# Kernel optimization log

Hardware: AMD Instinct MI355X
Metric: run time of the kernel (lower is better)

## Reference

```python
import jax, jax.numpy as jnp
import numpy as np

N = 100000   # nodes
E = 3200000  # edges
M = 4096     # moves
K = 16       # orders per move
NEG_SLOPE = 0.2  # PyG GATv2Conv default negative_slope

PARAM_SHAPES = {
    'g1_Wl': (10, 15), 'g1_Wr': (10, 15), 'g1_att': (10,), 'g1_b': (10,),
    'g2_Wl': (10, 25), 'g2_Wr': (10, 25), 'g2_att': (10,), 'g2_b': (10,),
    'g3_Wl': (10, 25), 'g3_Wr': (10, 25), 'g3_att': (10,), 'g3_b': (10,),
    'vt_W': (20, 29), 'vt_b': (20,), 'va_W': (1, 20), 'va_b': (1,),
    'vv_W': (10, 20), 'vv_b': (10,), 'vl_W': (1, 10), 'vl_b': (1,),
    'at_W': (20, 48), 'at_b': (20,), 'dt_W': (20, 23), 'dt_b': (20,),
    'oa_W': (1, 20), 'oa_b': (1,), 'ov_W': (1, 20), 'ov_b': (1,),
}
PARAM_NAMES = list(PARAM_SHAPES.keys())


def _linear(x, W, b):
    return x @ W.T + b


def _gatv2(x, src, dst, Wl, Wr, att, b):
    # GATv2Conv (heads=1, self-loops appended by caller), eval mode (no dropout)
    xl = x @ Wl.T  # messages from source nodes
    xr = x @ Wr.T
    e = (jax.nn.leaky_relu(xl[src] + xr[dst], NEG_SLOPE) * att).sum(-1)  # [E+N]
    emax = jax.ops.segment_max(e, dst, num_segments=N)
    ee = jnp.exp(e - emax[dst])
    denom = jax.ops.segment_sum(ee, dst, num_segments=N)
    alpha = ee / denom[dst]
    return jax.ops.segment_sum(alpha[:, None] * xl[src], dst, num_segments=N) + b


def _forward(x1, x2, edges, move_src, move_dst, move_armies, is_attack, params):
    (g1_Wl, g1_Wr, g1_att, g1_b,
     g2_Wl, g2_Wr, g2_att, g2_b,
     g3_Wl, g3_Wr, g3_att, g3_b,
     vt_W, vt_b, va_W, va_b, vv_W, vv_b, vl_W, vl_b,
     at_W, at_b, dt_W, dt_b, oa_W, oa_b, ov_W, ov_b) = params
    x2t = jnp.tile(x2, (N, 1))  # [N,4]
    self_idx = jnp.arange(N, dtype=edges.dtype)
    src = jnp.concatenate([edges[0], self_idx])
    dst = jnp.concatenate([edges[1], self_idx])
    x = jax.nn.relu(_gatv2(x1, src, dst, g1_Wl, g1_Wr, g1_att, g1_b))
    x = jax.nn.relu(_gatv2(jnp.concatenate([x, x1], 1), src, dst, g2_Wl, g2_Wr, g2_att, g2_b))
    x = jax.nn.relu(_gatv2(jnp.concatenate([x, x1], 1), src, dst, g3_Wl, g3_Wr, g3_att, g3_b))  # [N,10]
    # per-move order tensors (vectorized over [M,K]); deploy uses move_src as target
    xs, xd = x[move_src], x[move_dst]       # [M,K,10]
    x1s, x1d = x1[move_src], x1[move_dst]   # [M,K,15]
    extra = 0.6 * move_armies - 0.7 * (x1d[..., 3] + x1d[..., 4])
    attack_in = jnp.concatenate([xs, xd, x1s[..., 3:], x1d[..., 1:],
                                 move_armies[..., None], extra[..., None]], -1)  # [M,K,48]
    deploy_in = jnp.concatenate([xs, x1s[..., 3:], move_armies[..., None]], -1)  # [M,K,23]
    feat = jnp.where(is_attack[..., None] == 1,
                     _linear(attack_in, at_W, at_b),
                     _linear(deploy_in, dt_W, dt_b))
    feat = jax.nn.relu(feat)  # dropout = identity (eval)
    attn = jax.nn.softmax(_linear(feat, oa_W, oa_b), axis=1)  # softmax over orders
    p = (attn * _linear(feat, ov_W, ov_b)).sum(axis=(1, 2))   # [M]
    # value head: attention pooling over all nodes
    Vn = jax.nn.relu(_linear(jnp.concatenate([x, x1, x2t], 1), vt_W, vt_b))  # [N,20]
    vatt = jax.nn.softmax(_linear(Vn, va_W, va_b), axis=0)
    Vp = jax.nn.relu((vatt * _linear(Vn, vv_W, vv_b)).sum(axis=0))
    V = jnp.tanh(_linear(Vp, vl_W, vl_b))[0]
    return V, jax.nn.log_softmax(p, axis=0)


def setup_inputs() -> dict:
    key = jax.random.key(0)
    ks = iter(jax.random.split(key, 64))
    inp = {
        'x1': jax.random.normal(next(ks), (N, 15), jnp.float32),
        'x2': jax.random.normal(next(ks), (4,), jnp.float32),
        'edges': jax.random.randint(next(ks), (2, E), 0, N, jnp.int32),
        'move_src': jax.random.randint(next(ks), (M, K), 0, N, jnp.int32),
        'move_dst': jax.random.randint(next(ks), (M, K), 0, N, jnp.int32),
        'move_armies': jax.random.uniform(next(ks), (M, K), jnp.float32) * 10.0,
        'is_attack': jax.random.randint(next(ks), (M, K), 0, 2, jnp.int32),
    }
    for name, shape in PARAM_SHAPES.items():
        inp[name] = jax.random.normal(next(ks), shape, jnp.float32) * 0.1
    return inp


def reference(x1, x2, edges, move_src, move_dst, move_armies, is_attack,
              g1_Wl, g1_Wr, g1_att, g1_b, g2_Wl, g2_Wr, g2_att, g2_b,
              g3_Wl, g3_Wr, g3_att, g3_b, vt_W, vt_b, va_W, va_b,
              vv_W, vv_b, vl_W, vl_b, at_W, at_b, dt_W, dt_b,
              oa_W, oa_b, ov_W, ov_b):
    params = (g1_Wl, g1_Wr, g1_att, g1_b, g2_Wl, g2_Wr, g2_att, g2_b,
              g3_Wl, g3_Wr, g3_att, g3_b, vt_W, vt_b, va_W, va_b,
              vv_W, vv_b, vl_W, vl_b, at_W, at_b, dt_W, dt_b,
              oa_W, oa_b, ov_W, ov_b)
    return _forward(x1, x2, edges, move_src, move_dst, move_armies, is_attack, params)
```

## Files before the change

### kernel.cpp

```cpp
#include <hip/hip_runtime.h>
#include <hip/hip_bf16.h>
#include <hip/hip_fp16.h>
#include <math.h>

#define NN 100000
#define NE 3200000
#define MM 4096
#define KK 16
#define NEG_SLOPE 0.2f
#define SUB 8
#define BSH 8
#define NB 391
#define PCH 4096
#define FCAP 9728
#define XS 12
#define XSH 16

__device__ __forceinline__ void h10_to_f(const uint4& w0, unsigned w2, float* xs) {
    float2 f;
    f = __half22float2(*(const __half2*)&w0.x); xs[0]=f.x; xs[1]=f.y;
    f = __half22float2(*(const __half2*)&w0.y); xs[2]=f.x; xs[3]=f.y;
    f = __half22float2(*(const __half2*)&w0.z); xs[4]=f.x; xs[5]=f.y;
    f = __half22float2(*(const __half2*)&w0.w); xs[6]=f.x; xs[7]=f.y;
    f = __half22float2(*(const __half2*)&w2);   xs[8]=f.x; xs[9]=f.y;
}

__global__ __launch_bounds__(1024) void partition_kernel(const int* __restrict__ edges,
                                                         int* __restrict__ cnt,
                                                         unsigned* __restrict__ recs) {
    __shared__ unsigned rl[PCH];
    __shared__ unsigned srt[PCH];
    __shared__ unsigned short bb[PCH];
    __shared__ unsigned short bbs[PCH];
    __shared__ int h[NB];
    __shared__ int sc[1024];
    __shared__ int lb[NB];
    __shared__ int gb[NB];
    __shared__ int cur[NB];
    const int total = NE + NN;
    int base = blockIdx.x * PCH;
    int n = min(PCH, total - base);
    int t = threadIdx.x;
    if (t < NB) { h[t] = 0; cur[t] = 0; }
    __syncthreads();
    for (int j = t; j < n; j += 1024) {
        int i = base + j;
        int s, d;
        if (i < NE) { s = edges[i]; d = edges[NE + i]; }
        else        { s = i - NE; d = s; }
        rl[j] = ((unsigned)(d & 255) << 17) | (unsigned)s;
        int b = d >> BSH;
        bb[j] = (unsigned short)b;
        atomicAdd(&h[b], 1);
    }
    __syncthreads();
    int hv = (t < NB) ? h[t] : 0;
    sc[t] = hv;
    __syncthreads();
    for (int off = 1; off < 1024; off <<= 1) {
        int v = (t >= off) ? sc[t - off] : 0;
        __syncthreads();
        sc[t] += v;
        __syncthreads();
    }
    if (t < NB) {
        lb[t] = sc[t] - hv;
        if (hv > 0) gb[t] = atomicAdd(&cnt[t], hv);
    }
    __syncthreads();
    for (int j = t; j < n; j += 1024) {
        int b = bb[j];
        int l = atomicAdd(&cur[b], 1);
        int dst = lb[b] + l;
        srt[dst] = rl[j];
        bbs[dst] = (unsigned short)b;
    }
    __syncthreads();
    for (int j = t; j < n; j += 1024) {
        int b = bbs[j];
        int pos = gb[b] + (j - lb[b]);
        if (pos < FCAP) recs[(long)b * FCAP + pos] = srt[j];
    }
}

__global__ void bucket_scan_kernel(const int* __restrict__ cnt, int* __restrict__ bbase) {
    __shared__ int part[512];
    int t = threadIdx.x;
    int c = (t < NB) ? min(cnt[t], FCAP) : 0;
    part[t] = c;
    __syncthreads();
    for (int off = 1; off < 512; off <<= 1) {
        int v = (t >= off) ? part[t - off] : 0;
        __syncthreads();
        part[t] += v;
        __syncthreads();
    }
    if (t < NB) bbase[t] = part[t] - c;
    if (t == NB - 1) bbase[NB] = part[t];
}

__global__ __launch_bounds__(1024) void fine_sort_kernel(const unsigned* __restrict__ recs,
                                                         const int* __restrict__ cnt,
                                                         const int* __restrict__ bbase,
                                                         int* __restrict__ csr_src,
                                                         int* __restrict__ offsets) {
    __shared__ unsigned rl[FCAP];
    __shared__ int hist[256];
    __shared__ int sc[256];
    __shared__ int hb[257];
    __shared__ int cur[256];
    int b = blockIdx.x;
    int beg = bbase[b];
    int nb = min(cnt[b], FCAP);
    int t = threadIdx.x;
    int nodebase = b << BSH;
    int nnodes = min(256, NN - nodebase);
    if (t < 256) { hist[t] = 0; cur[t] = 0; }
    __syncthreads();
    const unsigned* rsrc = recs + (long)b * FCAP;
    for (int j = t; j < nb; j += 1024) {
        unsigned r = rsrc[j];
        rl[j] = r;
        atomicAdd(&hist[r >> 17], 1);
    }
    __syncthreads();
    int hv = (t < 256) ? hist[t] : 0;
    if (t < 256) sc[t] = hv;
    __syncthreads();
    for (int off = 1; off < 256; off <<= 1) {
        int v = 0;
        if (t < 256 && t >= off) v = sc[t - off];
        __syncthreads();
        if (t < 256) sc[t] += v;
        __syncthreads();
    }
    if (t < 256) hb[t] = sc[t] - hv;
    if (t == 0) hb[256] = nb;
    __syncthreads();
    for (int j = t; j < nb; j += 1024) {
        unsigned r = rl[j];
        int l = r >> 17;
        int p = hb[l] + atomicAdd(&cur[l], 1);
        csr_src[beg + p] = (int)(r & 0x1FFFFu);
    }
    if (t < nnodes) offsets[nodebase + t] = beg + hb[t];
    if (b == NB - 1 && t == 0) offsets[NN] = beg + nb;
}

__global__ void linear1_kernel(const float* __restrict__ x1,
                               const float* __restrict__ Wl,
                               const float* __restrict__ Wr,
                               __half* __restrict__ xlh,
                               float* __restrict__ xr) {
    int i = blockIdx.x * blockDim.x + threadIdx.x;
    if (i >= NN) return;
    float in[15];
    #pragma unroll
    for (int j = 0; j < 15; j++) in[j] = x1[i * 15 + j];
    float sl[10];
    #pragma unroll
    for (int o = 0; o < 10; o++) {
        float l = 0.f, r = 0.f;
        #pragma unroll
        for (int j = 0; j < 15; j++) {
            l += Wl[o * 15 + j] * in[j];
            r += Wr[o * 15 + j] * in[j];
        }
        sl[o] = l;
        xr[(long)i * XS + o] = r;
    }
    unsigned u[5];
    #pragma unroll
    for (int q = 0; q < 5; q++) {
        __half2 hh = __floats2half2_rn(sl[2*q], sl[2*q+1]);
        u[q] = *(unsigned*)&hh;
    }
    uint4* p4 = (uint4*)(xlh + (long)i * XSH);
    p4[0] = make_uint4(u[0], u[1], u[2], u[3]);
    *(uint2*)(xlh + (long)i * XSH + 8) = make_uint2(u[4], 0u);
}

template<bool FUSE_NEXT>
__global__ void gat_aggregate_kernel(const int* __restrict__ csr_src,
                                     const int* __restrict__ offsets,
                                     const __half* __restrict__ xlh,
                                     const float* __restrict__ xr,
                                     const float* __restrict__ att,
                                     const float* __restrict__ b,
                                     const float* __restrict__ x1,
                                     const float* __restrict__ nWl,
                                     const float* __restrict__ nWr,
                                     __half* __restrict__ xlo,
                                     float* __restrict__ xro,
                                     float* __restrict__ xout)
{
    int t = blockIdx.x * blockDim.x + threadIdx.x;
    int node = t / SUB;
    int lane = t % SUB;
    if (node >= NN) return;
    float xrn[12], a[10];
    const float4* xr4 = (const float4*)(xr + (long)node * XS);
    #pragma unroll
    for (int q = 0; q < 3; q++) {
        float4 v = xr4[q];
        xrn[4*q] = v.x; xrn[4*q+1] = v.y; xrn[4*q+2] = v.z; xrn[4*q+3] = v.w;
    }
    #pragma unroll
    for (int h = 0; h < 10; h++) a[h] = att[h];
    int beg = offsets[node], end = offsets[node + 1];
    float den = 0.f, num[10];
    #pragma unroll
    for (int h = 0; h < 10; h++) num[h] = 0.f;
    int j = beg + lane;
    for (; j + 3 * SUB < end; j += 4 * SUB) {
        int s0 = csr_src[j];
        int s1 = csr_src[j + SUB];
        int s2 = csr_src[j + 2 * SUB];
        int s3 = csr_src[j + 3 * SUB];
        const __half *p0 = xlh + (long)s0 * XSH, *p1 = xlh + (long)s1 * XSH;
        const __half *p2 = xlh + (long)s2 * XSH, *p3 = xlh + (long)s3 * XSH;
        uint4 w0a = *(const uint4*)p0; unsigned w0b = *(const unsigned*)(p0 + 8);
        uint4 w1a = *(const uint4*)p1; unsigned w1b = *(const unsigned*)(p1 + 8);
        uint4 w2a = *(const uint4*)p2; unsigned w2b = *(const unsigned*)(p2 + 8);
        uint4 w3a = *(const uint4*)p3; unsigned w3b = *(const unsigned*)(p3 + 8);
        uint4 wa[4] = {w0a, w1a, w2a, w3a};
        unsigned wb[4] = {w0b, w1b, w2b, w3b};
        #pragma unroll
        for (int q = 0; q < 4; q++) {
            float xs[10];
            h10_to_f(wa[q], wb[q], xs);
            float e = 0.f;
            #pragma unroll
            for (int h = 0; h < 10; h++) {
                float v = xs[h] + xrn[h];
                v = (v >= 0.f) ? v : NEG_SLOPE * v;
                e += v * a[h];
            }
            float w = __expf(e);
            den += w;
            #pragma unroll
            for (int h = 0; h < 10; h++) num[h] += w * xs[h];
        }
    }
    for (; j < end; j += SUB) {
        int s = csr_src[j];
        const __half* ph = xlh + (long)s * XSH;
        uint4 wa = *(const uint4*)ph;
        unsigned wb = *(const unsigned*)(ph + 8);
        float xs[10];
        h10_to_f(wa, wb, xs);
        float e = 0.f;
        #pragma unroll
        for (int h = 0; h < 10; h++) {
            float v = xs[h] + xrn[h];
            v = (v >= 0.f) ? v : NEG_SLOPE * v;
            e += v * a[h];
        }
        float w = __expf(e);
        den += w;
        #pragma unroll
        for (int h = 0; h < 10; h++) num[h] += w * xs[h];
    }
    #pragma unroll
    for (int off = SUB / 2; off; off >>= 1) {
        den += __shfl_xor(den, off, SUB);
        #pragma unroll
        for (int h = 0; h < 10; h++) num[h] += __shfl_xor(num[h], off, SUB);
    }
    float inv = 1.f / den;
    float xo[10];
    #pragma unroll
    for (int h = 0; h < 10; h++) xo[h] = fmaxf(num[h] * inv + b[h], 0.f);
    if (FUSE_NEXT) {
        if (lane < 5) {
            float in2[25];
            #pragma unroll
            for (int h = 0; h < 10; h++) in2[h] = xo[h];
            #pragma unroll
            for (int h = 0; h < 15; h++) in2[10 + h] = x1[(long)node * 15 + h];
            int o0 = 2 * lane, o1 = 2 * lane + 1;
            float sl0 = 0.f, sl1 = 0.f, sr0 = 0.f, sr1 = 0.f;
            #pragma unroll
            for (int jj = 0; jj < 25; jj++) {
                sl0 += nWl[o0 * 25 + jj] * in2[jj];
                sl1 += nWl[o1 * 25 + jj] * in2[jj];
                sr0 += nWr[o0 * 25 + jj] * in2[jj];
                sr1 += nWr[o1 * 25 + jj] * in2[jj];
            }
            __half2 hp = __floats2half2_rn(sl0, sl1);
            *(unsigned*)(xlo + (long)node * XSH + o0) = *(unsigned*)&hp;
            *(float2*)(xro + (long)node * XS + o0) = make_float2(sr0, sr1);
        }
    } else {
        if (lane == 0) {
            #pragma unroll
            for (int h = 0; h < 10; h++) xout[(long)node * XS + h] = xo[h];
        }
    }
}

__global__ void move_kernel(const float* __restrict__ x,
                            const float* __restrict__ x1,
                            const int* __restrict__ msrc,
                            const int* __restrict__ mdst,
                            const float* __restrict__ armies,
                            const int* __restrict__ isatk,
                            const float* __restrict__ at_W, const float* __restrict__ at_b,
                            const float* __restrict__ dt_W, const float* __restrict__ dt_b,
                            const float* __restrict__ oa_W, const float* __restrict__ oa_b,
                            const float* __restrict__ ov_W, const float* __restrict__ ov_b,
                            float* __restrict__ p) {
    int t = blockIdx.x * blockDim.x + threadIdx.x;
    int m = t >> 4;
    int k = t & 15;
    int s = msrc[t], d = mdst[t];
    float arm = armies[t];
    bool atk = (isatk[t] == 1);
    float xsrc[12];
    const float4* xs4 = (const float4*)(x + (long)s * XS);
    #pragma unroll
    for (int q = 0; q < 3; q++) {
        float4 v = xs4[q];
        xsrc[4*q] = v.x; xsrc[4*q+1] = v.y; xsrc[4*q+2] = v.z; xsrc[4*q+3] = v.w;
    }
    float feat[20];
    if (atk) {
        float in[48];
        #pragma unroll
        for (int h = 0; h < 10; h++) in[h] = xsrc[h];
        const float4* xd4 = (const float4*)(x + (long)d * XS);
        float xdst[12];
        #pragma unroll
        for (int q = 0; q < 3; q++) {
            float4 v = xd4[q];
            xdst[4*q] = v.x; xdst[4*q+1] = v.y; xdst[4*q+2] = v.z; xdst[4*q+3] = v.w;
        }
        #pragma unroll
        for (int h = 0; h < 10; h++) in[10 + h] = xdst[h];
        #pragma unroll
        for (int h = 0; h < 12; h++) in[20 + h] = x1[(long)s * 15 + 3 + h];
        #pragma unroll
        for (int h = 0; h < 14; h++) in[32 + h] = x1[(long)d * 15 + 1 + h];
        in[46] = arm;
        in[47] = 0.6f * arm - 0.7f * (x1[(long)d * 15 + 3] + x1[(long)d * 15 + 4]);
        #pragma unroll
        for (int o = 0; o < 20; o++) {
            float sum = at_b[o];
            #pragma unroll
            for (int j = 0; j < 48; j++) sum += at_W[o * 48 + j] * in[j];
            feat[o] = fmaxf(sum, 0.f);
        }
    } else {
        float in[23];
        #pragma unroll
        for (int h = 0; h < 10; h++) in[h] = xsrc[h];
        #pragma unroll
        for (int h = 0; h < 12; h++) in[10 + h] = x1[(long)s * 15 + 3 + h];
        in[22] = arm;
        #pragma unroll
        for (int o = 0; o < 20; o++) {
            float sum = dt_b[o];
            #pragma unroll
            for (int j = 0; j < 23; j++) sum += dt_W[o * 23 + j] * in[j];
            feat[o] = fmaxf(sum, 0.f);
        }
    }
    float oa = oa_b[0], ov = ov_b[0];
    #pragma unroll
    for (int j = 0; j < 20; j++) {
        oa += oa_W[j] * feat[j];
        ov += ov_W[j] * feat[j];
    }
    float mx = oa;
    #pragma unroll
    for (int off = 8; off; off >>= 1) mx = fmaxf(mx, __shfl_xor(mx, off, 16));
    float w = __expf(oa - mx);
    float nume = w * ov;
    float den = w;
    #pragma unroll
    for (int off = 8; off; off >>= 1) {
        nume += __shfl_xor(nume, off, 16);
        den  += __shfl_xor(den,  off, 16);
    }
    if (k == 0) p[m] = nume / den;
}

__global__ void logsoftmax_kernel(const float* __restrict__ p, float* __restrict__ out) {
    __shared__ float sm[256];
    int tid = threadIdx.x;
    float mx = -INFINITY;
    for (int i = tid; i < MM; i += 256) mx = fmaxf(mx, p[i]);
    sm[tid] = mx; __syncthreads();
    for (int s = 128; s; s >>= 1) { if (tid < s) sm[tid] = fmaxf(sm[tid], sm[tid + s]); __syncthreads(); }
    mx = sm[0]; __syncthreads();
    float sum = 0.f;
    for (int i = tid; i < MM; i += 256) sum += expf(p[i] - mx);
    sm[tid] = sum; __syncthreads();
    for (int s = 128; s; s >>= 1) { if (tid < s) sm[tid] += sm[tid + s]; __syncthreads(); }
    float ls = mx + logf(sm[0]);
    for (int i = tid; i < MM; i += 256) out[i] = p[i] - ls;
}

__global__ void value12_kernel(const float* __restrict__ x,
                               const float* __restrict__ x1,
                               const float* __restrict__ x2,
                               const float* __restrict__ vt_W, const float* __restrict__ vt_b,
                               const float* __restrict__ va_W, const float* __restrict__ va_b,
                               const float* __restrict__ vv_W, const float* __restrict__ vv_b,
                               float* __restrict__ partials) {
    __shared__ float sm[4][11];
    int i = blockIdx.x * blockDim.x + threadIdx.x;
    float w = 0.f;
    float acc[10];
    #pragma unroll
    for (int h = 0; h < 10; h++) acc[h] = 0.f;
    if (i < NN) {
        float in[29];
        const float4* xi4 = (const float4*)(x + (long)i * XS);
        float xi[12];
        #pragma unroll
        for (int q = 0; q < 3; q++) {
            float4 v = xi4[q];
            xi[4*q] = v.x; xi[4*q+1] = v.y; xi[4*q+2] = v.z; xi[4*q+3] = v.w;
        }
        #pragma unroll
        for (int h = 0; h < 10; h++) in[h] = xi[h];
        #pragma unroll
        for (int h = 0; h < 15; h++) in[10 + h] = x1[(long)i * 15 + h];
        #pragma unroll
        for (int h = 0; h < 4; h++) in[25 + h] = x2[h];
        float Vn[20];
        #pragma unroll
        for (int o = 0; o < 20; o++) {
            float s = vt_b[o];
            #pragma unroll
            for (int j = 0; j < 29; j++) s += vt_W[o * 29 + j] * in[j];
            Vn[o] = fmaxf(s, 0.f);
        }
        float lg = va_b[0];
        #pragma unroll
        for (int j = 0; j < 20; j++) lg += va_W[j] * Vn[j];
        w = __expf(lg);
        #pragma unroll
        for (int o = 0; o < 10; o++) {
            float s = vv_b[o];
            #pragma unroll
            for (int j = 0; j < 20; j++) s += vv_W[o * 20 + j] * Vn[j];
            acc[o] = w * s;
        }
    }
    #pragma unroll
    for (int off = 32; off; off >>= 1) {
        w += __shfl_xor(w, off, 64);
        #pragma unroll
        for (int h = 0; h < 10; h++) acc[h] += __shfl_xor(acc[h], off, 64);
    }
    int wid = threadIdx.x >> 6;
    if ((threadIdx.x & 63) == 0) {
        #pragma unroll
        for (int h = 0; h < 10; h++) sm[wid][h] = acc[h];
        sm[wid][10] = w;
    }
    __syncthreads();
    if (threadIdx.x < 11) {
        int c = threadIdx.x;
        partials[(long)blockIdx.x * 12 + c] = sm[0][c] + sm[1][c] + sm[2][c] + sm[3][c];
    }
}

__global__ void value3_kernel(const float* __restrict__ partials, int nparts,
                              const float* __restrict__ vl_W, const float* __restrict__ vl_b,
                              float* __restrict__ out0) {
    int lane = threadIdx.x;
    float s[11];
    #pragma unroll
    for (int c = 0; c < 11; c++) s[c] = 0.f;
    for (int j = lane; j < nparts; j += 64)
        #pragma unroll
        for (int c = 0; c < 11; c++) s[c] += partials[(long)j * 12 + c];
    #pragma unroll
    for (int off = 32; off; off >>= 1)
        #pragma unroll
        for (int c = 0; c < 11; c++) s[c] += __shfl_xor(s[c], off, 64);
    if (lane == 0) {
        float inv = 1.0f / s[10];
        float v = vl_b[0];
        #pragma unroll
        for (int h = 0; h < 10; h++) v += vl_W[h] * fmaxf(s[h] * inv, 0.f);
        out0[0] = tanhf(v);
    }
}

extern "C" void kernel_launch(void* const* d_in, const int* in_sizes, int n_in,
                              void* d_out, int out_size, void* d_ws, size_t ws_size,
                              hipStream_t stream) {
    const float* x1      = (const float*)d_in[0];
    const float* x2      = (const float*)d_in[1];
    const int*   edges   = (const int*)d_in[2];
    const int*   msrc    = (const int*)d_in[3];
    const int*   mdst    = (const int*)d_in[4];
    const float* armies  = (const float*)d_in[5];
    const int*   isatk   = (const int*)d_in[6];
    const float* g1_Wl = (const float*)d_in[7],  *g1_Wr = (const float*)d_in[8];
    const float* g1_att= (const float*)d_in[9],  *g1_b  = (const float*)d_in[10];
    const float* g2_Wl = (const float*)d_in[11], *g2_Wr = (const float*)d_in[12];
    const float* g2_att= (const float*)d_in[13], *g2_b  = (const float*)d_in[14];
    const float* g3_Wl = (const float*)d_in[15], *g3_Wr = (const float*)d_in[16];
    const float* g3_att= (const float*)d_in[17], *g3_b  = (const float*)d_in[18];
    const float* vt_W  = (const float*)d_in[19], *vt_b  = (const float*)d_in[20];
    const float* va_W  = (const float*)d_in[21], *va_b  = (const float*)d_in[22];
    const float* vv_W  = (const float*)d_in[23], *vv_b  = (const float*)d_in[24];
    const float* vl_W  = (const float*)d_in[25], *vl_b  = (const float*)d_in[26];
    const float* at_W  = (const float*)d_in[27], *at_b  = (const float*)d_in[28];
    const float* dt_W  = (const float*)d_in[29], *dt_b  = (const float*)d_in[30];
    const float* oa_W  = (const float*)d_in[31], *oa_b  = (const float*)d_in[32];
    const float* ov_W  = (const float*)d_in[33], *ov_b  = (const float*)d_in[34];

    float* out = (float*)d_out;

    float* ws = (float*)d_ws;
    __half* xlhA = (__half*)ws;
    __half* xlhB = xlhA + (long)NN * XSH;
    float* xrA = (float*)(xlhB + (long)NN * XSH);
    float* xrB = xrA + (long)NN * XS;
    float* xF  = xrB + (long)NN * XS;
    int* csr_src = (int*)(xF + (long)NN * XS);
    int* offsets = csr_src + (NE + NN);
    unsigned* recs = (unsigned*)(offsets + NN + 4);
    int* cnt   = (int*)(recs + (long)NB * FCAP);
    int* bbase = cnt + NB + 1;
    float* pbuf = (float*)(bbase + NB + 3);
    float* partials = pbuf + MM;

    const int nodeBlocks = (NN + 255) / 256;
    const int aggBlocks  = ((long)NN * SUB + 255) / 256;
    const int partBlocks = (NE + NN + PCH - 1) / PCH;

    hipMemsetAsync(cnt, 0, NB * sizeof(int), stream);
    partition_kernel<<<partBlocks, 1024, 0, stream>>>(edges, cnt, recs);
    bucket_scan_kernel<<<1, 512, 0, stream>>>(cnt, bbase);
    fine_sort_kernel<<<NB, 1024, 0, stream>>>(recs, cnt, bbase, csr_src, offsets);

    linear1_kernel<<<nodeBlocks, 256, 0, stream>>>(x1, g1_Wl, g1_Wr, xlhA, xrA);
    gat_aggregate_kernel<true><<<aggBlocks, 256, 0, stream>>>(
        csr_src, offsets, xlhA, xrA, g1_att, g1_b, x1, g2_Wl, g2_Wr, xlhB, xrB, nullptr);
    gat_aggregate_kernel<true><<<aggBlocks, 256, 0, stream>>>(
        csr_src, offsets, xlhB, xrB, g2_att, g2_b, x1, g3_Wl, g3_Wr, xlhA, xrA, nullptr);
    gat_aggregate_kernel<false><<<aggBlocks, 256, 0, stream>>>(
        csr_src, offsets, xlhA, xrA, g3_att, g3_b, x1, nullptr, nullptr, nullptr, nullptr, xF);

    move_kernel<<<(MM * KK) / 256, 256, 0, stream>>>(
        xF, x1, msrc, mdst, armies, isatk,
        at_W, at_b, dt_W, dt_b, oa_W, oa_b, ov_W, ov_b, pbuf);
    logsoftmax_kernel<<<1, 256, 0, stream>>>(pbuf, out + 1);

    value12_kernel<<<nodeBlocks, 256, 0, stream>>>(
        xF, x1, x2, vt_W, vt_b, va_W, va_b, vv_W, vv_b, partials);
    value3_kernel<<<1, 64, 0, stream>>>(partials, nodeBlocks, vl_W, vl_b, out);
}
```

Before: 377.7 us.

## Fuse all stages into one cooperative persistent kernel with grid syncs

Replaces the chain of separate kernel launches (partition, scan, fine sort, linear, three GAT aggregations, move scoring, log-softmax, value head) with a single cooperative mega-kernel. It uses grid-stride loops over a fixed grid and grid.sync between stages, and a shared-memory union reused across phases. The aim is to remove per-launch overhead and inter-kernel gaps. In exchange, parallelism is capped at 256 blocks of 1024 threads, the 1024-thread blocks may hurt occupancy in the aggregation phases, and each grid barrier costs time.

```diff
diff --git a/kernel.cpp b/kernel.cpp
--- a/kernel.cpp
+++ b/kernel.cpp
@@ -1,7 +1,9 @@
 #include <hip/hip_runtime.h>
-#include <hip/hip_bf16.h>
+#include <hip/hip_cooperative_groups.h>
 #include <hip/hip_fp16.h>
 #include <math.h>
+
+namespace cg = cooperative_groups;
 
 #define NN 100000
 #define NE 3200000
@@ -15,6 +17,38 @@
 #define FCAP 9728
 #define XS 12
 #define XSH 16
+#define GRID 256
+#define TPB 1024
+#define GSIZE (GRID * TPB)
+#define VPAD 100032
+
+struct KParams {
+    const float *x1, *x2;
+    const int *edges, *msrc, *mdst;
+    const float *armies; const int *isatk;
+    const float *g1_Wl, *g1_Wr, *g1_att, *g1_b;
+    const float *g2_Wl, *g2_Wr, *g2_att, *g2_b;
+    const float *g3_Wl, *g3_Wr, *g3_att, *g3_b;
+    const float *vt_W, *vt_b, *va_W, *va_b, *vv_W, *vv_b, *vl_W, *vl_b;
+    const float *at_W, *at_b, *dt_W, *dt_b, *oa_W, *oa_b, *ov_W, *ov_b;
+    __half *xlhA, *xlhB; float *xrA, *xrB, *xF;
+    int *csr_src, *offsets, *cnt, *bbase;
+    unsigned *recs;
+    float *pbuf, *partials, *out;
+};
+
+union SMem {
+    struct {
+        unsigned rl[PCH]; unsigned srt[PCH];
+        unsigned short bb[PCH]; unsigned short bbs[PCH];
+        int h[NB]; int sc[TPB]; int lb[NB]; int gb[NB]; int cur[NB];
+    } part;
+    struct {
+        unsigned rl[FCAP]; int hist[256]; int sc[256]; int hb[257]; int cur[256];
+    } fine;
+    struct { int part[TPB]; } scan;
+    struct { float sm[TPB]; } red;
+};
 
 __device__ __forceinline__ void h10_to_f(const uint4& w0, unsigned w2, float* xs) {
     float2 f;
@@ -25,210 +59,72 @@
     f = __half22float2(*(const __half2*)&w2);   xs[8]=f.x; xs[9]=f.y;
 }
 
-__global__ __launch_bounds__(1024) void partition_kernel(const int* __restrict__ edges,
-                                                         int* __restrict__ cnt,
-                                                         unsigned* __restrict__ recs) {
-    __shared__ unsigned rl[PCH];
-    __shared__ unsigned srt[PCH];
-    __shared__ unsigned short bb[PCH];
-    __shared__ unsigned short bbs[PCH];
-    __shared__ int h[NB];
-    __shared__ int sc[1024];
-    __shared__ int lb[NB];
-    __shared__ int gb[NB];
-    __shared__ int cur[NB];
-    const int total = NE + NN;
-    int base = blockIdx.x * PCH;
-    int n = min(PCH, total - base);
-    int t = threadIdx.x;
-    if (t < NB) { h[t] = 0; cur[t] = 0; }
-    __syncthreads();
-    for (int j = t; j < n; j += 1024) {
-        int i = base + j;
-        int s, d;
-        if (i < NE) { s = edges[i]; d = edges[NE + i]; }
-        else        { s = i - NE; d = s; }
-        rl[j] = ((unsigned)(d & 255) << 17) | (unsigned)s;
-        int b = d >> BSH;
-        bb[j] = (unsigned short)b;
-        atomicAdd(&h[b], 1);
-    }
-    __syncthreads();
-    int hv = (t < NB) ? h[t] : 0;
-    sc[t] = hv;
-    __syncthreads();
-    for (int off = 1; off < 1024; off <<= 1) {
-        int v = (t >= off) ? sc[t - off] : 0;
-        __syncthreads();
-        sc[t] += v;
-        __syncthreads();
-    }
-    if (t < NB) {
-        lb[t] = sc[t] - hv;
-        if (hv > 0) gb[t] = atomicAdd(&cnt[t], hv);
-    }
-    __syncthreads();
-    for (int j = t; j < n; j += 1024) {
-        int b = bb[j];
-        int l = atomicAdd(&cur[b], 1);
-        int dst = lb[b] + l;
-        srt[dst] = rl[j];
-        bbs[dst] = (unsigned short)b;
-    }
-    __syncthreads();
-    for (int j = t; j < n; j += 1024) {
-        int b = bbs[j];
-        int pos = gb[b] + (j - lb[b]);
-        if (pos < FCAP) recs[(long)b * FCAP + pos] = srt[j];
-    }
-}
-
-__global__ void bucket_scan_kernel(const int* __restrict__ cnt, int* __restrict__ bbase) {
-    __shared__ int part[512];
-    int t = threadIdx.x;
-    int c = (t < NB) ? min(cnt[t], FCAP) : 0;
-    part[t] = c;
-    __syncthreads();
-    for (int off = 1; off < 512; off <<= 1) {
-        int v = (t >= off) ? part[t - off] : 0;
-        __syncthreads();
-        part[t] += v;
-        __syncthreads();
-    }
-    if (t < NB) bbase[t] = part[t] - c;
-    if (t == NB - 1) bbase[NB] = part[t];
-}
-
-__global__ __launch_bounds__(1024) void fine_sort_kernel(const unsigned* __restrict__ recs,
-                                                         const int* __restrict__ cnt,
-                                                         const int* __restrict__ bbase,
-                                                         int* __restrict__ csr_src,
-                                                         int* __restrict__ offsets) {
-    __shared__ unsigned rl[FCAP];
-    __shared__ int hist[256];
-    __shared__ int sc[256];
-    __shared__ int hb[257];
-    __shared__ int cur[256];
-    int b = blockIdx.x;
-    int beg = bbase[b];
-    int nb = min(cnt[b], FCAP);
-    int t = threadIdx.x;
-    int nodebase = b << BSH;
-    int nnodes = min(256, NN - nodebase);
-    if (t < 256) { hist[t] = 0; cur[t] = 0; }
-    __syncthreads();
-    const unsigned* rsrc = recs + (long)b * FCAP;
-    for (int j = t; j < nb; j += 1024) {
-        unsigned r = rsrc[j];
-        rl[j] = r;
-        atomicAdd(&hist[r >> 17], 1);
-    }
-    __syncthreads();
-    int hv = (t < 256) ? hist[t] : 0;
-    if (t < 256) sc[t] = hv;
-    __syncthreads();
-    for (int off = 1; off < 256; off <<= 1) {
-        int v = 0;
-        if (t < 256 && t >= off) v = sc[t - off];
-        __syncthreads();
-        if (t < 256) sc[t] += v;
-        __syncthreads();
-    }
-    if (t < 256) hb[t] = sc[t] - hv;
-    if (t == 0) hb[256] = nb;
-    __syncthreads();
-    for (int j = t; j < nb; j += 1024) {
-        unsigned r = rl[j];
-        int l = r >> 17;
-        int p = hb[l] + atomicAdd(&cur[l], 1);
-        csr_src[beg + p] = (int)(r & 0x1FFFFu);
-    }
-    if (t < nnodes) offsets[nodebase + t] = beg + hb[t];
-    if (b == NB - 1 && t == 0) offsets[NN] = beg + nb;
-}
-
-__global__ void linear1_kernel(const float* __restrict__ x1,
-                               const float* __restrict__ Wl,
-                               const float* __restrict__ Wr,
-                               __half* __restrict__ xlh,
-                               float* __restrict__ xr) {
-    int i = blockIdx.x * blockDim.x + threadIdx.x;
-    if (i >= NN) return;
-    float in[15];
-    #pragma unroll
-    for (int j = 0; j < 15; j++) in[j] = x1[i * 15 + j];
-    float sl[10];
-    #pragma unroll
-    for (int o = 0; o < 10; o++) {
-        float l = 0.f, r = 0.f;
-        #pragma unroll
-        for (int j = 0; j < 15; j++) {
-            l += Wl[o * 15 + j] * in[j];
-            r += Wr[o * 15 + j] * in[j];
-        }
-        sl[o] = l;
-        xr[(long)i * XS + o] = r;
-    }
-    unsigned u[5];
-    #pragma unroll
-    for (int q = 0; q < 5; q++) {
-        __half2 hh = __floats2half2_rn(sl[2*q], sl[2*q+1]);
-        u[q] = *(unsigned*)&hh;
-    }
-    uint4* p4 = (uint4*)(xlh + (long)i * XSH);
-    p4[0] = make_uint4(u[0], u[1], u[2], u[3]);
-    *(uint2*)(xlh + (long)i * XSH + 8) = make_uint2(u[4], 0u);
-}
-
-template<bool FUSE_NEXT>
-__global__ void gat_aggregate_kernel(const int* __restrict__ csr_src,
-                                     const int* __restrict__ offsets,
-                                     const __half* __restrict__ xlh,
-                                     const float* __restrict__ xr,
-                                     const float* __restrict__ att,
-                                     const float* __restrict__ b,
-                                     const float* __restrict__ x1,
-                                     const float* __restrict__ nWl,
-                                     const float* __restrict__ nWr,
-                                     __half* __restrict__ xlo,
-                                     float* __restrict__ xro,
-                                     float* __restrict__ xout)
-{
-    int t = blockIdx.x * blockDim.x + threadIdx.x;
-    int node = t / SUB;
-    int lane = t % SUB;
-    if (node >= NN) return;
-    float xrn[12], a[10];
-    const float4* xr4 = (const float4*)(xr + (long)node * XS);
-    #pragma unroll
-    for (int q = 0; q < 3; q++) {
-        float4 v = xr4[q];
-        xrn[4*q] = v.x; xrn[4*q+1] = v.y; xrn[4*q+2] = v.z; xrn[4*q+3] = v.w;
-    }
-    #pragma unroll
-    for (int h = 0; h < 10; h++) a[h] = att[h];
-    int beg = offsets[node], end = offsets[node + 1];
-    float den = 0.f, num[10];
-    #pragma unroll
-    for (int h = 0; h < 10; h++) num[h] = 0.f;
-    int j = beg + lane;
-    for (; j + 3 * SUB < end; j += 4 * SUB) {
-        int s0 = csr_src[j];
-        int s1 = csr_src[j + SUB];
-        int s2 = csr_src[j + 2 * SUB];
-        int s3 = csr_src[j + 3 * SUB];
-        const __half *p0 = xlh + (long)s0 * XSH, *p1 = xlh + (long)s1 * XSH;
-        const __half *p2 = xlh + (long)s2 * XSH, *p3 = xlh + (long)s3 * XSH;
-        uint4 w0a = *(const uint4*)p0; unsigned w0b = *(const unsigned*)(p0 + 8);
-        uint4 w1a = *(const uint4*)p1; unsigned w1b = *(const unsigned*)(p1 + 8);
-        uint4 w2a = *(const uint4*)p2; unsigned w2b = *(const unsigned*)(p2 + 8);
-        uint4 w3a = *(const uint4*)p3; unsigned w3b = *(const unsigned*)(p3 + 8);
-        uint4 wa[4] = {w0a, w1a, w2a, w3a};
-        unsigned wb[4] = {w0b, w1b, w2b, w3b};
-        #pragma unroll
-        for (int q = 0; q < 4; q++) {
+template<bool FUSE>
+__device__ void aggregate_phase(const KParams& P,
+                                const __half* __restrict__ xlh,
+                                const float* __restrict__ xr,
+                                const float* __restrict__ att,
+                                const float* __restrict__ bias,
+                                const float* __restrict__ nWl,
+                                const float* __restrict__ nWr,
+                                __half* __restrict__ xlo,
+                                float* __restrict__ xro,
+                                float* __restrict__ xout,
+                                int tid) {
+    for (long wk = tid; wk < (long)NN * SUB; wk += GSIZE) {
+        int node = (int)(wk >> 3);
+        int lane = (int)(wk & 7);
+        float xrn[12], a[10];
+        const float4* xr4 = (const float4*)(xr + (long)node * XS);
+        #pragma unroll
+        for (int q = 0; q < 3; q++) {
+            float4 v = xr4[q];
+            xrn[4*q]=v.x; xrn[4*q+1]=v.y; xrn[4*q+2]=v.z; xrn[4*q+3]=v.w;
+        }
+        #pragma unroll
+        for (int h = 0; h < 10; h++) a[h] = att[h];
+        int beg = P.offsets[node], end = P.offsets[node + 1];
+        float den = 0.f, num[10];
+        #pragma unroll
+        for (int h = 0; h < 10; h++) num[h] = 0.f;
+        int j = beg + lane;
+        for (; j + 3 * SUB < end; j += 4 * SUB) {
+            int s0 = P.csr_src[j];
+            int s1 = P.csr_src[j + SUB];
+            int s2 = P.csr_src[j + 2 * SUB];
+            int s3 = P.csr_src[j + 3 * SUB];
+            const __half *p0 = xlh + (long)s0 * XSH, *p1 = xlh + (long)s1 * XSH;
+            const __half *p2 = xlh + (long)s2 * XSH, *p3 = xlh + (long)s3 * XSH;
+            uint4 w0a = *(const uint4*)p0; unsigned w0b = *(const unsigned*)(p0 + 8);
+            uint4 w1a = *(const uint4*)p1; unsigned w1b = *(const unsigned*)(p1 + 8);
+            uint4 w2a = *(const uint4*)p2; unsigned w2b = *(const unsigned*)(p2 + 8);
+            uint4 w3a = *(const uint4*)p3; unsigned w3b = *(const unsigned*)(p3 + 8);
+            uint4 wa[4] = {w0a, w1a, w2a, w3a};
+            unsigned wb[4] = {w0b, w1b, w2b, w3b};
+            #pragma unroll
+            for (int q = 0; q < 4; q++) {
+                float xs[10];
+                h10_to_f(wa[q], wb[q], xs);
+                float e = 0.f;
+                #pragma unroll
+                for (int h = 0; h < 10; h++) {
+                    float v = xs[h] + xrn[h];
+                    v = (v >= 0.f) ? v : NEG_SLOPE * v;
+                    e += v * a[h];
+                }
+                float w = __expf(e);
+                den += w;
+                #pragma unroll
+                for (int h = 0; h < 10; h++) num[h] += w * xs[h];
+            }
+        }
+        for (; j < end; j += SUB) {
+            int s = P.csr_src[j];
+            const __half* ph = xlh + (long)s * XSH;
+            uint4 wa = *(const uint4*)ph;
+            unsigned wb = *(const unsigned*)(ph + 8);
             float xs[10];
-            h10_to_f(wa[q], wb[q], xs);
+            h10_to_f(wa, wb, xs);
             float e = 0.f;
             #pragma unroll
             for (int h = 0; h < 10; h++) {
@@ -241,320 +137,411 @@
             #pragma unroll
             for (int h = 0; h < 10; h++) num[h] += w * xs[h];
         }
-    }
-    for (; j < end; j += SUB) {
-        int s = csr_src[j];
-        const __half* ph = xlh + (long)s * XSH;
-        uint4 wa = *(const uint4*)ph;
-        unsigned wb = *(const unsigned*)(ph + 8);
-        float xs[10];
-        h10_to_f(wa, wb, xs);
-        float e = 0.f;
-        #pragma unroll
-        for (int h = 0; h < 10; h++) {
-            float v = xs[h] + xrn[h];
-            v = (v >= 0.f) ? v : NEG_SLOPE * v;
-            e += v * a[h];
-        }
-        float w = __expf(e);
-        den += w;
-        #pragma unroll
-        for (int h = 0; h < 10; h++) num[h] += w * xs[h];
-    }
-    #pragma unroll
-    for (int off = SUB / 2; off; off >>= 1) {
-        den += __shfl_xor(den, off, SUB);
-        #pragma unroll
-        for (int h = 0; h < 10; h++) num[h] += __shfl_xor(num[h], off, SUB);
-    }
-    float inv = 1.f / den;
-    float xo[10];
-    #pragma unroll
-    for (int h = 0; h < 10; h++) xo[h] = fmaxf(num[h] * inv + b[h], 0.f);
-    if (FUSE_NEXT) {
-        if (lane < 5) {
-            float in2[25];
-            #pragma unroll
-            for (int h = 0; h < 10; h++) in2[h] = xo[h];
-            #pragma unroll
-            for (int h = 0; h < 15; h++) in2[10 + h] = x1[(long)node * 15 + h];
-            int o0 = 2 * lane, o1 = 2 * lane + 1;
-            float sl0 = 0.f, sl1 = 0.f, sr0 = 0.f, sr1 = 0.f;
-            #pragma unroll
-            for (int jj = 0; jj < 25; jj++) {
-                sl0 += nWl[o0 * 25 + jj] * in2[jj];
-                sl1 += nWl[o1 * 25 + jj] * in2[jj];
-                sr0 += nWr[o0 * 25 + jj] * in2[jj];
-                sr1 += nWr[o1 * 25 + jj] * in2[jj];
-            }
-            __half2 hp = __floats2half2_rn(sl0, sl1);
-            *(unsigned*)(xlo + (long)node * XSH + o0) = *(unsigned*)&hp;
-            *(float2*)(xro + (long)node * XS + o0) = make_float2(sr0, sr1);
-        }
-    } else {
-        if (lane == 0) {
-            #pragma unroll
-            for (int h = 0; h < 10; h++) xout[(long)node * XS + h] = xo[h];
+        #pragma unroll
+        for (int off = SUB / 2; off; off >>= 1) {
+            den += __shfl_xor(den, off, SUB);
+            #pragma unroll
+            for (int h = 0; h < 10; h++) num[h] += __shfl_xor(num[h], off, SUB);
+        }
+        float inv = 1.f / den;
+        float xo[10];
+        #pragma unroll
+        for (int h = 0; h < 10; h++) xo[h] = fmaxf(num[h] * inv + bias[h], 0.f);
+        if (FUSE) {
+            if (lane < 5) {
+                float in2[25];
+                #pragma unroll
+                for (int h = 0; h < 10; h++) in2[h] = xo[h];
+                #pragma unroll
+                for (int h = 0; h < 15; h++) in2[10 + h] = P.x1[(long)node * 15 + h];
+                int o0 = 2 * lane, o1 = 2 * lane + 1;
+                float sl0 = 0.f, sl1 = 0.f, sr0 = 0.f, sr1 = 0.f;
+                #pragma unroll
+                for (int jj = 0; jj < 25; jj++) {
+                    sl0 += nWl[o0 * 25 + jj] * in2[jj];
+                    sl1 += nWl[o1 * 25 + jj] * in2[jj];
+                    sr0 += nWr[o0 * 25 + jj] * in2[jj];
+                    sr1 += nWr[o1 * 25 + jj] * in2[jj];
+                }
+                __half2 hp = __floats2half2_rn(sl0, sl1);
+                *(unsigned*)(xlo + (long)node * XSH + o0) = *(unsigned*)&hp;
+                *(float2*)(xro + (long)node * XS + o0) = make_float2(sr0, sr1);
+            }
+        } else {
+            if (lane == 0) {
+                #pragma unroll
+                for (int h = 0; h < 10; h++) xout[(long)node * XS + h] = xo[h];
+            }
         }
     }
 }
 
-__global__ void move_kernel(const float* __restrict__ x,
-                            const float* __restrict__ x1,
-                            const int* __restrict__ msrc,
-                            const int* __restrict__ mdst,
-                            const float* __restrict__ armies,
-                            const int* __restrict__ isatk,
-                            const float* __restrict__ at_W, const float* __restrict__ at_b,
-                            const float* __restrict__ dt_W, const float* __restrict__ dt_b,
-                            const float* __restrict__ oa_W, const float* __restrict__ oa_b,
-                            const float* __restrict__ ov_W, const float* __restrict__ ov_b,
-                            float* __restrict__ p) {
-    int t = blockIdx.x * blockDim.x + threadIdx.x;
-    int m = t >> 4;
-    int k = t & 15;
-    int s = msrc[t], d = mdst[t];
-    float arm = armies[t];
-    bool atk = (isatk[t] == 1);
-    float xsrc[12];
-    const float4* xs4 = (const float4*)(x + (long)s * XS);
-    #pragma unroll
-    for (int q = 0; q < 3; q++) {
-        float4 v = xs4[q];
-        xsrc[4*q] = v.x; xsrc[4*q+1] = v.y; xsrc[4*q+2] = v.z; xsrc[4*q+3] = v.w;
+__global__ __launch_bounds__(TPB, 4) void mega_kernel(KParams P) {
+    cg::grid_group grid = cg::this_grid();
+    __shared__ SMem sm;
+    int t = threadIdx.x;
+    int tid = blockIdx.x * TPB + t;
+
+    for (int i = tid; i < NB; i += GSIZE) P.cnt[i] = 0;
+    grid.sync();
+
+    {
+        const int total = NE + NN;
+        const int nchunks = (total + PCH - 1) / PCH;
+        for (int c = blockIdx.x; c < nchunks; c += GRID) {
+            int base = c * PCH;
+            int n = min(PCH, total - base);
+            if (t < NB) { sm.part.h[t] = 0; sm.part.cur[t] = 0; }
+            __syncthreads();
+            for (int j = t; j < n; j += TPB) {
+                int i = base + j;
+                int s, d;
+                if (i < NE) { s = P.edges[i]; d = P.edges[NE + i]; }
+                else        { s = i - NE; d = s; }
+                sm.part.rl[j] = ((unsigned)(d & 255) << 17) | (unsigned)s;
+                int b = d >> BSH;
+                sm.part.bb[j] = (unsigned short)b;
+                atomicAdd(&sm.part.h[b], 1);
+            }
+            __syncthreads();
+            int hv = (t < NB) ? sm.part.h[t] : 0;
+            sm.part.sc[t] = hv;
+            __syncthreads();
+            for (int off = 1; off < TPB; off <<= 1) {
+                int v = (t >= off) ? sm.part.sc[t - off] : 0;
+                __syncthreads();
+                sm.part.sc[t] += v;
+                __syncthreads();
+            }
+            if (t < NB) {
+                sm.part.lb[t] = sm.part.sc[t] - hv;
+                if (hv > 0) sm.part.gb[t] = atomicAdd(&P.cnt[t], hv);
+            }
+            __syncthreads();
+            for (int j = t; j < n; j += TPB) {
+                int b = sm.part.bb[j];
+                int l = atomicAdd(&sm.part.cur[b], 1);
+                int dst = sm.part.lb[b] + l;
+                sm.part.srt[dst] = sm.part.rl[j];
+                sm.part.bbs[dst] = (unsigned short)b;
+            }
+            __syncthreads();
+            for (int j = t; j < n; j += TPB) {
+                int b = sm.part.bbs[j];
+                int pos = sm.part.gb[b] + (j - sm.part.lb[b]);
+                if (pos < FCAP) P.recs[(long)b * FCAP + pos] = sm.part.srt[j];
+            }
+            __syncthreads();
+        }
     }
-    float feat[20];
-    if (atk) {
-        float in[48];
-        #pragma unroll
-        for (int h = 0; h < 10; h++) in[h] = xsrc[h];
-        const float4* xd4 = (const float4*)(x + (long)d * XS);
-        float xdst[12];
+    grid.sync();
+
+    if (blockIdx.x == 0) {
+        int c = (t < NB) ? min(P.cnt[t], FCAP) : 0;
+        sm.scan.part[t] = c;
+        __syncthreads();
+        for (int off = 1; off < TPB; off <<= 1) {
+            int v = (t >= off) ? sm.scan.part[t - off] : 0;
+            __syncthreads();
+            sm.scan.part[t] += v;
+            __syncthreads();
+        }
+        if (t < NB) P.bbase[t] = sm.scan.part[t] - c;
+        if (t == NB - 1) P.bbase[NB] = sm.scan.part[t];
+    } else {
+        for (int i = (blockIdx.x - 1) * TPB + t; i < NN; i += (GRID - 1) * TPB) {
+            float in[15];
+            #pragma unroll
+            for (int j = 0; j < 15; j++) in[j] = P.x1[(long)i * 15 + j];
+            float sl[10];
+            #pragma unroll
+            for (int o = 0; o < 10; o++) {
+                float l = 0.f, r = 0.f;
+                #pragma unroll
+                for (int j = 0; j < 15; j++) {
+                    l += P.g1_Wl[o * 15 + j] * in[j];
+                    r += P.g1_Wr[o * 15 + j] * in[j];
+                }
+                sl[o] = l;
+                P.xrA[(long)i * XS + o] = r;
+            }
+            unsigned u[5];
+            #pragma unroll
+            for (int q = 0; q < 5; q++) {
+                __half2 hh = __floats2half2_rn(sl[2*q], sl[2*q+1]);
+                u[q] = *(unsigned*)&hh;
+            }
+            uint4* p4 = (uint4*)(P.xlhA + (long)i * XSH);
+            p4[0] = make_uint4(u[0], u[1], u[2], u[3]);
+            *(uint2*)(P.xlhA + (long)i * XSH + 8) = make_uint2(u[4], 0u);
+        }
+    }
+    grid.sync();
+
+    for (int b = blockIdx.x; b < NB; b += GRID) {
+        int beg = P.bbase[b];
+        int nb = min(P.cnt[b], FCAP);
+        int nodebase = b << BSH;
+        int nnodes = min(256, NN - nodebase);
+        if (t < 256) { sm.fine.hist[t] = 0; sm.fine.cur[t] = 0; }
+        __syncthreads();
+        const unsigned* rsrc = P.recs + (long)b * FCAP;
+        for (int j = t; j < nb; j += TPB) {
+            unsigned r = rsrc[j];
+            sm.fine.rl[j] = r;
+            atomicAdd(&sm.fine.hist[r >> 17], 1);
+        }
+        __syncthreads();
+        int hv = (t < 256) ? sm.fine.hist[t] : 0;
+        if (t < 256) sm.fine.sc[t] = hv;
+        __syncthreads();
+        for (int off = 1; off < 256; off <<= 1) {
+            int v = 0;
+            if (t < 256 && t >= off) v = sm.fine.sc[t - off];
+            __syncthreads();
+            if (t < 256) sm.fine.sc[t] += v;
+            __syncthreads();
+        }
+        if (t < 256) sm.fine.hb[t] = sm.fine.sc[t] - hv;
+        if (t == 0) sm.fine.hb[256] = nb;
+        __syncthreads();
+        for (int j = t; j < nb; j += TPB) {
+            unsigned r = sm.fine.rl[j];
+            int l = r >> 17;
+            int p = sm.fine.hb[l] + atomicAdd(&sm.fine.cur[l], 1);
+            P.csr_src[beg + p] = (int)(r & 0x1FFFFu);
+        }
+        if (t < nnodes) P.offsets[nodebase + t] = beg + sm.fine.hb[t];
+        if (b == NB - 1 && t == 0) P.offsets[NN] = beg + nb;
+        __syncthreads();
+    }
+    grid.sync();
+
+    aggregate_phase<true>(P, P.xlhA, P.xrA, P.g1_att, P.g1_b,
+                          P.g2_Wl, P.g2_Wr, P.xlhB, P.xrB, nullptr, tid);
+    grid.sync();
+    aggregate_phase<true>(P, P.xlhB, P.xrB, P.g2_att, P.g2_b,
+                          P.g3_Wl, P.g3_Wr, P.xlhA, P.xrA, nullptr, tid);
+    grid.sync();
+    aggregate_phase<false>(P, P.xlhA, P.xrA, P.g3_att, P.g3_b,
+                           nullptr, nullptr, nullptr, nullptr, P.xF, tid);
+    grid.sync();
+
+    if (tid < MM * KK) {
+        int mt = tid;
+        int m = mt >> 4;
+        int k = mt & 15;
+        int s = P.msrc[mt], d = P.mdst[mt];
+        float arm = P.armies[mt];
+        bool atk = (P.isatk[mt] == 1);
+        float xsrc[12];
+        const float4* xs4 = (const float4*)(P.xF + (long)s * XS);
         #pragma unroll
         for (int q = 0; q < 3; q++) {
-            float4 v = xd4[q];
-            xdst[4*q] = v.x; xdst[4*q+1] = v.y; xdst[4*q+2] = v.z; xdst[4*q+3] = v.w;
-        }
-        #pragma unroll
-        for (int h = 0; h < 10; h++) in[10 + h] = xdst[h];
-        #pragma unroll
-        for (int h = 0; h < 12; h++) in[20 + h] = x1[(long)s * 15 + 3 + h];
-        #pragma unroll
-        for (int h = 0; h < 14; h++) in[32 + h] = x1[(long)d * 15 + 1 + h];
-        in[46] = arm;
-        in[47] = 0.6f * arm - 0.7f * (x1[(long)d * 15 + 3] + x1[(long)d * 15 + 4]);
-        #pragma unroll
-        for (int o = 0; o < 20; o++) {
-            float sum = at_b[o];
-            #pragma unroll
-            for (int j = 0; j < 48; j++) sum += at_W[o * 48 + j] * in[j];
-            feat[o] = fmaxf(sum, 0.f);
-        }
-    } else {
-        float in[23];
-        #pragma unroll
-        for (int h = 0; h < 10; h++) in[h] = xsrc[h];
-        #pragma unroll
-        for (int h = 0; h < 12; h++) in[10 + h] = x1[(long)s * 15 + 3 + h];
-        in[22] = arm;
-        #pragma unroll
-        for (int o = 0; o < 20; o++) {
-            float sum = dt_b[o];
-            #pragma unroll
-            for (int j = 0; j < 23; j++) sum += dt_W[o * 23 + j] * in[j];
-            feat[o] = fmaxf(sum, 0.f);
+            float4 v = xs4[q];
+            xsrc[4*q]=v.x; xsrc[4*q+1]=v.y; xsrc[4*q+2]=v.z; xsrc[4*q+3]=v.w;
+        }
+        float feat[20];
+        if (atk) {
+            float in[48];
+            #pragma unroll
+            for (int h = 0; h < 10; h++) in[h] = xsrc[h];
+            const float4* xd4 = (const float4*)(P.xF + (long)d * XS);
+            float xdst[12];
+            #pragma unroll
+            for (int q = 0; q < 3; q++) {
+                float4 v = xd4[q];
+                xdst[4*q]=v.x; xdst[4*q+1]=v.y; xdst[4*q+2]=v.z; xdst[4*q+3]=v.w;
+            }
+            #pragma unroll
+            for (int h = 0; h < 10; h++) in[10 + h] = xdst[h];
+            #pragma unroll
+            for (int h = 0; h < 12; h++) in[20 + h] = P.x1[(long)s * 15 + 3 + h];
+            #pragma unroll
+            for (int h = 0; h < 14; h++) in[32 + h] = P.x1[(long)d * 15 + 1 + h];
+            in[46] = arm;
+            in[47] = 0.6f * arm - 0.7f * (P.x1[(long)d * 15 + 3] + P.x1[(long)d * 15 + 4]);
+            #pragma unroll
+            for (int o = 0; o < 20; o++) {
+                float sum = P.at_b[o];
+                #pragma unroll
+                for (int j = 0; j < 48; j++) sum += P.at_W[o * 48 + j] * in[j];
+                feat[o] = fmaxf(sum, 0.f);
+            }
+        } else {
+            float in[23];
+            #pragma unroll
+            for (int h = 0; h < 10; h++) in[h] = xsrc[h];
+            #pragma unroll
+            for (int h = 0; h < 12; h++) in[10 + h] = P.x1[(long)s * 15 + 3 + h];
+            in[22] = arm;
+            #pragma unroll
+            for (int o = 0; o < 20; o++) {
+                float sum = P.dt_b[o];
+                #pragma unroll
+                for (int j = 0; j < 23; j++) sum += P.dt_W[o * 23 + j] * in[j];
+                feat[o] = fmaxf(sum, 0.f);
+            }
+        }
+        float oa = P.oa_b[0], ov = P.ov_b[0];
+        #pragma unroll
+        for (int j = 0; j < 20; j++) {
+            oa += P.oa_W[j] * feat[j];
+            ov += P.ov_W[j] * feat[j];
+        }
+        float mx = oa;
+        #pragma unroll
+        for (int off = 8; off; off >>= 1) mx = fmaxf(mx, __shfl_xor(mx, off, 16));
+        float w = __expf(oa - mx);
+        float nume = w * ov;
+        float den = w;
+        #pragma unroll
+        for (int off = 8; off; off >>= 1) {
+            nume += __shfl_xor(nume, off, 16);
+            den  += __shfl_xor(den,  off, 16);
+        }
+        if (k == 0) P.pbuf[m] = nume / den;
+    } else if (tid < MM * KK + VPAD) {
+        int i = tid - MM * KK;
+        float w = 0.f;
+        float acc[10];
+        #pragma unroll
+        for (int h = 0; h < 10; h++) acc[h] = 0.f;
+        if (i < NN) {
+            float in[29];
+            const float4* xi4 = (const float4*)(P.xF + (long)i * XS);
+            float xi[12];
+            #pragma unroll
+            for (int q = 0; q < 3; q++) {
+                float4 v = xi4[q];
+                xi[4*q]=v.x; xi[4*q+1]=v.y; xi[4*q+2]=v.z; xi[4*q+3]=v.w;
+            }
+            #pragma unroll
+            for (int h = 0; h < 10; h++) in[h] = xi[h];
+            #pragma unroll
+            for (int h = 0; h < 15; h++) in[10 + h] = P.x1[(long)i * 15 + h];
+            #pragma unroll
+            for (int h = 0; h < 4; h++) in[25 + h] = P.x2[h];
+            float Vn[20];
+            #pragma unroll
+            for (int o = 0; o < 20; o++) {
+                float s = P.vt_b[o];
+                #pragma unroll
+                for (int j = 0; j < 29; j++) s += P.vt_W[o * 29 + j] * in[j];
+                Vn[o] = fmaxf(s, 0.f);
+            }
+            float lg = P.va_b[0];
+            #pragma unroll
+            for (int j = 0; j < 20; j++) lg += P.va_W[j] * Vn[j];
+            w = __expf(lg);
+            #pragma unroll
+            for (int o = 0; o < 10; o++) {
+                float s = P.vv_b[o];
+                #pragma unroll
+                for (int j = 0; j < 20; j++) s += P.vv_W[o * 20 + j] * Vn[j];
+                acc[o] = w * s;
+            }
+        }
+        #pragma unroll
+        for (int off = 32; off; off >>= 1) {
+            w += __shfl_xor(w, off, 64);
+            #pragma unroll
+            for (int h = 0; h < 10; h++) acc[h] += __shfl_xor(acc[h], off, 64);
+        }
+        if ((i & 63) == 0) {
+            int wv = i >> 6;
+            #pragma unroll
+            for (int h = 0; h < 10; h++) P.partials[(long)wv * 12 + h] = acc[h];
+            P.partials[(long)wv * 12 + 10] = w;
         }
     }
-    float oa = oa_b[0], ov = ov_b[0];
-    #pragma unroll
-    for (int j = 0; j < 20; j++) {
-        oa += oa_W[j] * feat[j];
-        ov += ov_W[j] * feat[j];
-    }
-    float mx = oa;
-    #pragma unroll
-    for (int off = 8; off; off >>= 1) mx = fmaxf(mx, __shfl_xor(mx, off, 16));
-    float w = __expf(oa - mx);
-    float nume = w * ov;
-    float den = w;
-    #pragma unroll
-    for (int off = 8; off; off >>= 1) {
-        nume += __shfl_xor(nume, off, 16);
-        den  += __shfl_xor(den,  off, 16);
-    }
-    if (k == 0) p[m] = nume / den;
-}
-
-__global__ void logsoftmax_kernel(const float* __restrict__ p, float* __restrict__ out) {
-    __shared__ float sm[256];
-    int tid = threadIdx.x;
-    float mx = -INFINITY;
-    for (int i = tid; i < MM; i += 256) mx = fmaxf(mx, p[i]);
-    sm[tid] = mx; __syncthreads();
-    for (int s = 128; s; s >>= 1) { if (tid < s) sm[tid] = fmaxf(sm[tid], sm[tid + s]); __syncthreads(); }
-    mx = sm[0]; __syncthreads();
-    float sum = 0.f;
-    for (int i = tid; i < MM; i += 256) sum += expf(p[i] - mx);
-    sm[tid] = sum; __syncthreads();
-    for (int s = 128; s; s >>= 1) { if (tid < s) sm[tid] += sm[tid + s]; __syncthreads(); }
-    float ls = mx + logf(sm[0]);
-    for (int i = tid; i < MM; i += 256) out[i] = p[i] - ls;
-}
-
-__global__ void value12_kernel(const float* __restrict__ x,
-                               const float* __restrict__ x1,
-                               const float* __restrict__ x2,
-                               const float* __restrict__ vt_W, const float* __restrict__ vt_b,
-                               const float* __restrict__ va_W, const float* __restrict__ va_b,
-                               const float* __restrict__ vv_W, const float* __restrict__ vv_b,
-                               float* __restrict__ partials) {
-    __shared__ float sm[4][11];
-    int i = blockIdx.x * blockDim.x + threadIdx.x;
-    float w = 0.f;
-    float acc[10];
-    #pragma unroll
-    for (int h = 0; h < 10; h++) acc[h] = 0.f;
-    if (i < NN) {
-        float in[29];
-        const float4* xi4 = (const float4*)(x + (long)i * XS);
-        float xi[12];
-        #pragma unroll
-        for (int q = 0; q < 3; q++) {
-            float4 v = xi4[q];
-            xi[4*q] = v.x; xi[4*q+1] = v.y; xi[4*q+2] = v.z; xi[4*q+3] = v.w;
-        }
-        #pragma unroll
-        for (int h = 0; h < 10; h++) in[h] = xi[h];
-        #pragma unroll
-        for (int h = 0; h < 15; h++) in[10 + h] = x1[(long)i * 15 + h];
-        #pragma unroll
-        for (int h = 0; h < 4; h++) in[25 + h] = x2[h];
-        float Vn[20];
-        #pragma unroll
-        for (int o = 0; o < 20; o++) {
-            float s = vt_b[o];
-            #pragma unroll
-            for (int j = 0; j < 29; j++) s += vt_W[o * 29 + j] * in[j];
-            Vn[o] = fmaxf(s, 0.f);
-        }
-        float lg = va_b[0];
-        #pragma unroll
-        for (int j = 0; j < 20; j++) lg += va_W[j] * Vn[j];
-        w = __expf(lg);
-        #pragma unroll
-        for (int o = 0; o < 10; o++) {
-            float s = vv_b[o];
-            #pragma unroll
-            for (int j = 0; j < 20; j++) s += vv_W[o * 20 + j] * Vn[j];
-            acc[o] = w * s;
-        }
-    }
-    #pragma unroll
-    for (int off = 32; off; off >>= 1) {
-        w += __shfl_xor(w, off, 64);
-        #pragma unroll
-        for (int h = 0; h < 10; h++) acc[h] += __shfl_xor(acc[h], off, 64);
-    }
-    int wid = threadIdx.x >> 6;
-    if ((threadIdx.x & 63) == 0) {
-        #pragma unroll
-        for (int h = 0; h < 10; h++) sm[wid][h] = acc[h];
-        sm[wid][10] = w;
-    }
-    __syncthreads();
-    if (threadIdx.x < 11) {
-        int c = threadIdx.x;
-        partials[(long)blockIdx.x * 12 + c] = sm[0][c] + sm[1][c] + sm[2][c] + sm[3][c];
-    }
-}
-
-__global__ void value3_kernel(const float* __restrict__ partials, int nparts,
-                              const float* __restrict__ vl_W, const float* __restrict__ vl_b,
-                              float* __restrict__ out0) {
-    int lane = threadIdx.x;
-    float s[11];
-    #pragma unroll
-    for (int c = 0; c < 11; c++) s[c] = 0.f;
-    for (int j = lane; j < nparts; j += 64)
-        #pragma unroll
-        for (int c = 0; c < 11; c++) s[c] += partials[(long)j * 12 + c];
-    #pragma unroll
-    for (int off = 32; off; off >>= 1)
-        #pragma unroll
-        for (int c = 0; c < 11; c++) s[c] += __shfl_xor(s[c], off, 64);
-    if (lane == 0) {
-        float inv = 1.0f / s[10];
-        float v = vl_b[0];
-        #pragma unroll
-        for (int h = 0; h < 10; h++) v += vl_W[h] * fmaxf(s[h] * inv, 0.f);
-        out0[0] = tanhf(v);
+    grid.sync();
+
+    if (blockIdx.x == 0) {
+        float mx = -INFINITY;
+        for (int i = t; i < MM; i += TPB) mx = fmaxf(mx, P.pbuf[i]);
+        sm.red.sm[t] = mx;
+        __syncthreads();
+        for (int s = 512; s; s >>= 1) {
+            if (t < s) sm.red.sm[t] = fmaxf(sm.red.sm[t], sm.red.sm[t + s]);
+            __syncthreads();
+        }
+        mx = sm.red.sm[0];
+        __syncthreads();
+        float sum = 0.f;
+        for (int i = t; i < MM; i += TPB) sum += expf(P.pbuf[i] - mx);
+        sm.red.sm[t] = sum;
+        __syncthreads();
+        for (int s = 512; s; s >>= 1) {
+            if (t < s) sm.red.sm[t] += sm.red.sm[t + s];
+            __syncthreads();
+        }
+        float ls = mx + logf(sm.red.sm[0]);
+        for (int i = t; i < MM; i += TPB) P.out[1 + i] = P.pbuf[i] - ls;
+    } else if (blockIdx.x == 1 && t < 64) {
+        const int nparts = VPAD / 64;
+        float s[11];
+        #pragma unroll
+        for (int c = 0; c < 11; c++) s[c] = 0.f;
+        for (int j = t; j < nparts; j += 64)
+            #pragma unroll
+            for (int c = 0; c < 11; c++) s[c] += P.partials[(long)j * 12 + c];
+        #pragma unroll
+        for (int off = 32; off; off >>= 1)
+            #pragma unroll
+            for (int c = 0; c < 11; c++) s[c] += __shfl_xor(s[c], off, 64);
+        if (t == 0) {
+            float inv = 1.0f / s[10];
+            float v = P.vl_b[0];
+            #pragma unroll
+            for (int h = 0; h < 10; h++) v += P.vl_W[h] * fmaxf(s[h] * inv, 0.f);
+            P.out[0] = tanhf(v);
+        }
     }
 }
 
 extern "C" void kernel_launch(void* const* d_in, const int* in_sizes, int n_in,
                               void* d_out, int out_size, void* d_ws, size_t ws_size,
                               hipStream_t stream) {
-    const float* x1      = (const float*)d_in[0];
-    const float* x2      = (const float*)d_in[1];
-    const int*   edges   = (const int*)d_in[2];
-    const int*   msrc    = (const int*)d_in[3];
-    const int*   mdst    = (const int*)d_in[4];
-    const float* armies  = (const float*)d_in[5];
-    const int*   isatk   = (const int*)d_in[6];
-    const float* g1_Wl = (const float*)d_in[7],  *g1_Wr = (const float*)d_in[8];
-    const float* g1_att= (const float*)d_in[9],  *g1_b  = (const float*)d_in[10];
-    const float* g2_Wl = (const float*)d_in[11], *g2_Wr = (const float*)d_in[12];
-    const float* g2_att= (const float*)d_in[13], *g2_b  = (const float*)d_in[14];
-    const float* g3_Wl = (const float*)d_in[15], *g3_Wr = (const float*)d_in[16];
-    const float* g3_att= (const float*)d_in[17], *g3_b  = (const float*)d_in[18];
-    const float* vt_W  = (const float*)d_in[19], *vt_b  = (const float*)d_in[20];
-    const float* va_W  = (const float*)d_in[21], *va_b  = (const float*)d_in[22];
-    const float* vv_W  = (const float*)d_in[23], *vv_b  = (const float*)d_in[24];
-    const float* vl_W  = (const float*)d_in[25], *vl_b  = (const float*)d_in[26];
-    const float* at_W  = (const float*)d_in[27], *at_b  = (const float*)d_in[28];
-    const float* dt_W  = (const float*)d_in[29], *dt_b  = (const float*)d_in[30];
-    const float* oa_W  = (const float*)d_in[31], *oa_b  = (const float*)d_in[32];
-    const float* ov_W  = (const float*)d_in[33], *ov_b  = (const float*)d_in[34];
-
-    float* out = (float*)d_out;
+    KParams P;
+    P.x1     = (const float*)d_in[0];
+    P.x2     = (const float*)d_in[1];
+    P.edges  = (const int*)d_in[2];
+    P.msrc   = (const int*)d_in[3];
+    P.mdst   = (const int*)d_in[4];
+    P.armies = (const float*)d_in[5];
+    P.isatk  = (const int*)d_in[6];
+    P.g1_Wl = (const float*)d_in[7];  P.g1_Wr = (const float*)d_in[8];
+    P.g1_att= (const float*)d_in[9];  P.g1_b  = (const float*)d_in[10];
+    P.g2_Wl = (const float*)d_in[11]; P.g2_Wr = (const float*)d_in[12];
+    P.g2_att= (const float*)d_in[13]; P.g2_b  = (const float*)d_in[14];
+    P.g3_Wl = (const float*)d_in[15]; P.g3_Wr = (const float*)d_in[16];
+    P.g3_att= (const float*)d_in[17]; P.g3_b  = (const float*)d_in[18];
+    P.vt_W  = (const float*)d_in[19]; P.vt_b  = (const float*)d_in[20];
+    P.va_W  = (const float*)d_in[21]; P.va_b  = (const float*)d_in[22];
+    P.vv_W  = (const float*)d_in[23]; P.vv_b  = (const float*)d_in[24];
+    P.vl_W  = (const float*)d_in[25]; P.vl_b  = (const float*)d_in[26];
+    P.at_W  = (const float*)d_in[27]; P.at_b  = (const float*)d_in[28];
+    P.dt_W  = (const float*)d_in[29]; P.dt_b  = (const float*)d_in[30];
+    P.oa_W  = (const float*)d_in[31]; P.oa_b  = (const float*)d_in[32];
+    P.ov_W  = (const float*)d_in[33]; P.ov_b  = (const float*)d_in[34];
+    P.out   = (float*)d_out;
 
     float* ws = (float*)d_ws;
-    __half* xlhA = (__half*)ws;
-    __half* xlhB = xlhA + (long)NN * XSH;
-    float* xrA = (float*)(xlhB + (long)NN * XSH);
-    float* xrB = xrA + (long)NN * XS;
-    float* xF  = xrB + (long)NN * XS;
-    int* csr_src = (int*)(xF + (long)NN * XS);
-    int* offsets = csr_src + (NE + NN);
-    unsigned* recs = (unsigned*)(offsets + NN + 4);
-    int* cnt   = (int*)(recs + (long)NB * FCAP);
-    int* bbase = cnt + NB + 1;
-    float* pbuf = (float*)(bbase + NB + 3);
-    float* partials = pbuf + MM;
-
-    const int nodeBlocks = (NN + 255) / 256;
-    const int aggBlocks  = ((long)NN * SUB + 255) / 256;
-    const int partBlocks = (NE + NN + PCH - 1) / PCH;
-
-    hipMemsetAsync(cnt, 0, NB * sizeof(int), stream);
-    partition_kernel<<<partBlocks, 1024, 0, stream>>>(edges, cnt, recs);
-    bucket_scan_kernel<<<1, 512, 0, stream>>>(cnt, bbase);
-    fine_sort_kernel<<<NB, 1024, 0, stream>>>(recs, cnt, bbase, csr_src, offsets);
-
-    linear1_kernel<<<nodeBlocks, 256, 0, stream>>>(x1, g1_Wl, g1_Wr, xlhA, xrA);
-    gat_aggregate_kernel<true><<<aggBlocks, 256, 0, stream>>>(
-        csr_src, offsets, xlhA, xrA, g1_att, g1_b, x1, g2_Wl, g2_Wr, xlhB, xrB, nullptr);
-    gat_aggregate_kernel<true><<<aggBlocks, 256, 0, stream>>>(
-        csr_src, offsets, xlhB, xrB, g2_att, g2_b, x1, g3_Wl, g3_Wr, xlhA, xrA, nullptr);
-    gat_aggregate_kernel<false><<<aggBlocks, 256, 0, stream>>>(
-        csr_src, offsets, xlhA, xrA, g3_att, g3_b, x1, nullptr, nullptr, nullptr, nullptr, xF);
-
-    move_kernel<<<(MM * KK) / 256, 256, 0, stream>>>(
-        xF, x1, msrc, mdst, armies, isatk,
-        at_W, at_b, dt_W, dt_b, oa_W, oa_b, ov_W, ov_b, pbuf);
-    logsoftmax_kernel<<<1, 256, 0, stream>>>(pbuf, out + 1);
-
-    value12_kernel<<<nodeBlocks, 256, 0, stream>>>(
-        xF, x1, x2, vt_W, vt_b, va_W, va_b, vv_W, vv_b, partials);
-    value3_kernel<<<1, 64, 0, stream>>>(partials, nodeBlocks, vl_W, vl_b, out);
+    P.xlhA = (__half*)ws;
+    P.xlhB = P.xlhA + (long)NN * XSH;
+    P.xrA  = (float*)(P.xlhB + (long)NN * XSH);
+    P.xrB  = P.xrA + (long)NN * XS;
+    P.xF   = P.xrB + (long)NN * XS;
+    P.csr_src = (int*)(P.xF + (long)NN * XS);
+    P.offsets = P.csr_src + (NE + NN);
+    P.recs = (unsigned*)(P.offsets + NN + 4);
+    P.cnt  = (int*)(P.recs + (long)NB * FCAP);
+    P.bbase = P.cnt + NB + 1;
+    P.pbuf = (float*)(P.bbase + NB + 3);
+    P.partials = P.pbuf + MM;
+
+    void* kargs[] = { (void*)&P };
+    hipLaunchCooperativeKernel((const void*)mega_kernel, dim3(GRID), dim3(TPB),
+                               kargs, 0, stream);
 }
```

After: 722.2 us. 91.2% more time.
